# Kernel optimization log

Hardware: AMD Instinct MI355X
Metric: run time of the kernel (lower is better)

The kernel has to match this reference:

```python
import jax, jax.numpy as jnp
import numpy as np

B, S, D, H = 4, 2048, 1024, 16
HD = D // H

def setup_inputs() -> dict:
    key = jax.random.key(0)
    ks = jax.random.split(key, 12)
    std = 1.0 / np.sqrt(D)
    inp = {
        'query': jax.random.normal(ks[0], (B, S, D), jnp.float32),
        'key':   jax.random.normal(ks[1], (B, S, D), jnp.float32),
        'value': jax.random.normal(ks[2], (B, S, D), jnp.float32),
        'mask':  jnp.tril(jnp.ones((S, S), jnp.int32))[None, None, :, :],  # [1,1,S,S] causal
        'Wq': jax.random.uniform(ks[3], (D, D), jnp.float32, -std, std),
        'bq': jax.random.uniform(ks[4], (D,), jnp.float32, -std, std),
        'Wk': jax.random.uniform(ks[5], (D, D), jnp.float32, -std, std),
        'bk': jax.random.uniform(ks[6], (D,), jnp.float32, -std, std),
        'Wv': jax.random.uniform(ks[7], (D, D), jnp.float32, -std, std),
        'bv': jax.random.uniform(ks[8], (D,), jnp.float32, -std, std),
        'Wo': jax.random.uniform(ks[9], (D, D), jnp.float32, -std, std),
        'bo': jax.random.uniform(ks[10], (D,), jnp.float32, -std, std),
    }
    return inp

def _split_heads(x, W, b):
    # torch Linear: x @ W.T + b ; then [B,S,H,HD] -> [B,H,S,HD]
    y = jnp.einsum('bsd,ed->bse', x, W) + b
    return y.reshape(x.shape[0], -1, H, HD).transpose(0, 2, 1, 3)

def reference(query, key, value, mask, Wq, bq, Wk, bk, Wv, bv, Wo, bo):
    q = _split_heads(query, Wq, bq)   # [B,H,S,HD]
    k = _split_heads(key,   Wk, bk)
    v = _split_heads(value, Wv, bv)
    logits = jnp.einsum('bhqd,bhkd->bhqk', q, k) / np.sqrt(HD)  # [B,H,S,S]
    logits = jnp.where(mask == 0, jnp.float32(-1e9), logits)
    attn = jax.nn.softmax(logits, axis=-1)
    out = jnp.einsum('bhqk,bhkd->bhqd', attn, v)               # [B,H,S,HD]
    out = out.transpose(0, 2, 1, 3).reshape(query.shape[0], -1, D)
    return jnp.einsum('bsd,ed->bse', out, Wo) + bo
```

## Files before the change

kernel.cpp:

```cpp
#include <hip/hip_runtime.h>
#include <hip/hip_bf16.h>


#define SLEN 2048
#define DMOD 1024

typedef __attribute__((ext_vector_type(8))) short s16x8;
typedef __attribute__((ext_vector_type(4))) float f32x4;

__device__ __forceinline__ unsigned short f2bf(float f) {
    union { __hip_bfloat16 h; unsigned short u; } cv;
    cv.h = __float2bfloat16(f);
    return cv.u;
}
__device__ __forceinline__ unsigned pack2bf(float a, float b) {
    return (unsigned)f2bf(a) | ((unsigned)f2bf(b) << 16);
}

__device__ __forceinline__ void gload_lds16(const void* g, void* l) {
    __builtin_amdgcn_global_load_lds(
        (const __attribute__((address_space(1))) void*)g,
        (__attribute__((address_space(3))) void*)l, 16, 0, 0);
}

__global__ __launch_bounds__(256) void convert_bf16(
    const float* __restrict__ q, const float* __restrict__ k,
    const float* __restrict__ v, const float* __restrict__ wq,
    const float* __restrict__ wk, const float* __restrict__ wv,
    const float* __restrict__ wo, unsigned short* __restrict__ ws)
{
    const int bid = blockIdx.x, tid = threadIdx.x;
    const float* src;
    unsigned short* dst;
    size_t off;
    if (bid < 3072) {
        const int t = bid >> 10;
        src = (t == 0) ? q : (t == 1) ? k : v;
        dst = ws + (size_t)t * 8388608;
        off = (size_t)(bid & 1023) * 8192;
    } else {
        const int w = (bid - 3072) >> 7;
        src = (w == 0) ? wq : (w == 1) ? wk : (w == 2) ? wv : wo;
        dst = ws + 25165824 + (size_t)w * 1048576;
        off = (size_t)((bid - 3072) & 127) * 8192;
    }
#pragma unroll
    for (int i = 0; i < 8; ++i) {
        const size_t e = off + (size_t)(i * 256 + tid) * 4;
        float4 x = *reinterpret_cast<const float4*>(&src[e]);
        uint2 u;
        u.x = pack2bf(x.x, x.y);
        u.y = pack2bf(x.z, x.w);
        *reinterpret_cast<uint2*>(&dst[e]) = u;
    }
}

template<int MODE>
__global__ __launch_bounds__(256) void gemm_bf16(
    const unsigned short* __restrict__ A, const unsigned short* __restrict__ W,
    const float* __restrict__ bias, void* __restrict__ outp)
{
    __shared__ unsigned short Asm[128 * 64];
    __shared__ unsigned short Bsm[128 * 64];

    const int tid  = threadIdx.x;
    const int lane = tid & 63, wid = tid >> 6;
    const int l15 = lane & 15, lhi = lane >> 4;

    const int flat = blockIdx.x;
    const int logical = (flat & 7) * 64 + (flat >> 3);
    const int m0 = (logical >> 3) * 128, n0 = (logical & 7) * 128;

    const int wr = wid >> 1, wc = wid & 1;
    const int srow = lane >> 3;
    const int sgr  = (lane & 7) ^ srow;

    f32x4 acc[4][4];
#pragma unroll
    for (int i = 0; i < 4; ++i)
#pragma unroll
        for (int j = 0; j < 4; ++j) acc[i][j] = (f32x4)0.f;

#pragma unroll 1
    for (int k0 = 0; k0 < 1024; k0 += 64) {
#pragma unroll
        for (int i = 0; i < 4; ++i) {
            const int rl = i * 32 + wid * 8 + srow;
            gload_lds16(&A[(size_t)(m0 + rl) * 1024 + k0 + sgr * 8],
                        (char*)Asm + i * 4096 + wid * 1024);
            gload_lds16(&W[(size_t)(n0 + rl) * 1024 + k0 + sgr * 8],
                        (char*)Bsm + i * 4096 + wid * 1024);
        }
        __syncthreads();

#pragma unroll
        for (int kk = 0; kk < 2; ++kk) {
            s16x8 af[4], bfv[4];
#pragma unroll
            for (int i = 0; i < 4; ++i) {
                const int row = wr * 64 + i * 16 + l15;
                const int s = (4 * kk + lhi) ^ (l15 & 7);
                af[i] = *reinterpret_cast<const s16x8*>(&Asm[row * 64 + s * 8]);
            }
#pragma unroll
            for (int j = 0; j < 4; ++j) {
                const int row = wc * 64 + j * 16 + l15;
                const int s = (4 * kk + lhi) ^ (l15 & 7);
                bfv[j] = *reinterpret_cast<const s16x8*>(&Bsm[row * 64 + s * 8]);
            }
#pragma unroll
            for (int i = 0; i < 4; ++i)
#pragma unroll
                for (int j = 0; j < 4; ++j)
                    acc[i][j] = __builtin_amdgcn_mfma_f32_16x16x32_bf16(af[i], bfv[j], acc[i][j], 0, 0, 0);
        }
        __syncthreads();
    }

#pragma unroll
    for (int j = 0; j < 4; ++j) {
        const int col = n0 + wc * 64 + j * 16 + l15;
        const float bv = bias[col];
#pragma unroll
        for (int i = 0; i < 4; ++i) {
#pragma unroll
            for (int r = 0; r < 4; ++r) {
                const int row = m0 + wr * 64 + i * 16 + lhi * 4 + r;
                const float val = acc[i][j][r] + bv;
                if constexpr (MODE == 2) {
                    ((float*)outp)[(size_t)row * 1024 + col] = val;
                } else if constexpr (MODE == 0) {
                    ((unsigned short*)outp)[(size_t)((row >> 11) * 16 + (col >> 6)) * 131072
                                            + (size_t)(row & 2047) * 64 + (col & 63)] = f2bf(val);
                } else {
                    ((unsigned short*)outp)[(size_t)((row >> 11) * 16 + (col >> 6)) * 131072
                                            + (size_t)(col & 63) * 2048 + (row & 2047)] = f2bf(val);
                }
            }
        }
    }
}

#define EXPC 0.18033688011112043f

__global__ __launch_bounds__(256, 4) void attn_kernel(
    const unsigned short* __restrict__ Q,
    const unsigned short* __restrict__ Kc,
    const unsigned short* __restrict__ Vt,
    unsigned short* __restrict__ Ao)
{
    __shared__ unsigned short Kbuf[2][4096];
    __shared__ unsigned short Vbuf[2][4096];
    __shared__ unsigned short Psm[4][1024];

    const int tid = threadIdx.x, lane = tid & 63, wid = tid >> 6;
    const int l15 = lane & 15, lhi = lane >> 4;
    const int sK = l15 & 7;
    const int sub = lane >> 3, c8s = lane & 7;

    const int flat = blockIdx.x;
    const int logical = (flat & 7) * 128 + (flat >> 3);
    const int bx = logical & 15, bh = logical >> 4;

    const size_t base = (size_t)bh * SLEN * 64;
    const unsigned short* Qb = Q + base;
    const unsigned short* Kb = Kc + base;
    const unsigned short* Vb = Vt + base;
    const int b = bh >> 4, h = bh & 15;

#pragma unroll 1
    for (int seg = 0; seg < 2; ++seg) {
        const int qt = seg ? (31 - bx) : bx;
        const int q0 = qt * 64;
        const int qrow = q0 + wid * 16 + l15;

        s16x8 aq[2];
#pragma unroll
        for (int kk = 0; kk < 2; ++kk)
            aq[kk] = *reinterpret_cast<const s16x8*>(
                &Qb[(size_t)(q0 + wid * 16 + l15) * 64 + kk * 32 + 8 * lhi]);

        f32x4 o_acc[4];
#pragma unroll
        for (int nb = 0; nb < 4; ++nb) o_acc[nb] = (f32x4)0.f;
        float m_r = -1e30f, l_part = 0.f;

        const int nt = qt + 1;

        auto stage = [&](int tt, int bsel) {
#pragma unroll
            for (int i = 0; i < 2; ++i) {
                const int row = 16 * wid + 8 * i + sub;
                const int col16 = c8s ^ (row & 7);
                gload_lds16(&Kb[(size_t)(tt * 64 + row) * 64 + col16 * 8],
                            (char*)&Kbuf[bsel][0] + wid * 2048 + i * 1024);
                gload_lds16(&Vb[(size_t)row * SLEN + tt * 64 + col16 * 8],
                            (char*)&Vbuf[bsel][0] + wid * 2048 + i * 1024);
            }
        };

        stage(0, 0);
        __syncthreads();

        int cur = 0;
#pragma unroll 1
        for (int t = 0; t < nt; ++t) {
            const int kv0 = t * 64;
            if (t + 1 < nt) stage(t + 1, cur ^ 1);

            const unsigned short* KL = Kbuf[cur];
            const unsigned short* VL = Vbuf[cur];

            f32x4 sc2[4];
#pragma unroll
            for (int nb = 0; nb < 4; ++nb) sc2[nb] = (f32x4)0.f;
            __builtin_amdgcn_s_setprio(1);
#pragma unroll
            for (int kk = 0; kk < 2; ++kk) {
                s16x8 ak[4];
#pragma unroll
                for (int nb = 0; nb < 4; ++nb) {
                    const int g = (nb * 16 + l15) * 8 + ((4 * kk + lhi) ^ sK);
                    ak[nb] = *reinterpret_cast<const s16x8*>(&KL[g * 8]);
                }
#pragma unroll
                for (int nb = 0; nb < 4; ++nb)
                    sc2[nb] = __builtin_amdgcn_mfma_f32_16x16x32_bf16(ak[nb], aq[kk], sc2[nb], 0, 0, 0);
            }
            __builtin_amdgcn_s_setprio(0);

            const bool diag = (kv0 + 63 > q0 + wid * 16);
            float tmx = -3e30f;
#pragma unroll
            for (int nb = 0; nb < 4; ++nb)
#pragma unroll
                for (int r = 0; r < 4; ++r) {
                    float x = sc2[nb][r];
                    if (diag && (kv0 + nb * 16 + lhi * 4 + r > qrow)) x = -3e30f;
                    sc2[nb][r] = x;
                    tmx = fmaxf(tmx, x);
                }

            if (__any(tmx - m_r > 64.0f)) {
                float tf = fmaxf(tmx, __shfl_xor(tmx, 16));
                tf = fmaxf(tf, __shfl_xor(tf, 32));
                const float mn = fmaxf(m_r, tf);
                const float alpha = exp2f((m_r - mn) * EXPC);
                m_r = mn;
                l_part *= alpha;
                float ar[4];
#pragma unroll
                for (int r = 0; r < 4; ++r) ar[r] = __shfl(alpha, lhi * 4 + r);
#pragma unroll
                for (int nb = 0; nb < 4; ++nb)
#pragma unroll
                    for (int r = 0; r < 4; ++r) o_acc[nb][r] *= ar[r];
            }

            const float negmC = -m_r * EXPC;
            unsigned short* Pw = &Psm[wid][0];
#pragma unroll
            for (int nb = 0; nb < 4; ++nb) {
                float p0 = exp2f(fmaf(sc2[nb][0], EXPC, negmC));
                float p1 = exp2f(fmaf(sc2[nb][1], EXPC, negmC));
                float p2 = exp2f(fmaf(sc2[nb][2], EXPC, negmC));
                float p3 = exp2f(fmaf(sc2[nb][3], EXPC, negmC));
                l_part += (p0 + p1) + (p2 + p3);
                uint2 u;
                u.x = pack2bf(p0, p1);
                u.y = pack2bf(p2, p3);
                const int g8 = l15 * 16 + ((nb * 4 + lhi) ^ (2 * sK));
                *reinterpret_cast<uint2*>(&Pw[g8 * 4]) = u;
            }

            __builtin_amdgcn_s_setprio(1);
#pragma unroll
            for (int kk = 0; kk < 2; ++kk) {
                const int gp = l15 * 8 + ((4 * kk + lhi) ^ sK);
                s16x8 pa = *reinterpret_cast<const s16x8*>(&Pw[gp * 8]);
                s16x8 bvv[4];
#pragma unroll
                for (int nb = 0; nb < 4; ++nb) {
                    const int g = (nb * 16 + l15) * 8 + ((4 * kk + lhi) ^ sK);
                    bvv[nb] = *reinterpret_cast<const s16x8*>(&VL[g * 8]);
                }
#pragma unroll
                for (int nb = 0; nb < 4; ++nb)
                    o_acc[nb] = __builtin_amdgcn_mfma_f32_16x16x32_bf16(pa, bvv[nb], o_acc[nb], 0, 0, 0);
            }
            __builtin_amdgcn_s_setprio(0);

            __syncthreads();
            cur ^= 1;
        }

        float lf = l_part + __shfl_xor(l_part, 16);
        lf += __shfl_xor(lf, 32);
        float linv[4];
#pragma unroll
        for (int r = 0; r < 4; ++r)
            linv[r] = 1.0f / __shfl(lf, lhi * 4 + r);
#pragma unroll
        for (int nb = 0; nb < 4; ++nb)
#pragma unroll
            for (int r = 0; r < 4; ++r) {
                const int s = q0 + wid * 16 + lhi * 4 + r;
                Ao[((size_t)b * SLEN + s) * DMOD + h * 64 + nb * 16 + l15] =
                    f2bf(o_acc[nb][r] * linv[r]);
            }
        if (seg == 0) __syncthreads();
    }
}

extern "C" void kernel_launch(void* const* d_in, const int* in_sizes, int n_in,
                              void* d_out, int out_size, void* d_ws, size_t ws_size,
                              hipStream_t stream) {
    const float* q  = (const float*)d_in[0];
    const float* k  = (const float*)d_in[1];
    const float* v  = (const float*)d_in[2];
    const float* Wq = (const float*)d_in[4];
    const float* bq = (const float*)d_in[5];
    const float* Wk = (const float*)d_in[6];
    const float* bk = (const float*)d_in[7];
    const float* Wv = (const float*)d_in[8];
    const float* bv = (const float*)d_in[9];
    const float* Wo = (const float*)d_in[10];
    const float* bo = (const float*)d_in[11];

    unsigned short* wsp = (unsigned short*)d_ws;
    unsigned short* qc  = wsp;
    unsigned short* kc  = wsp + 8388608;
    unsigned short* vc  = wsp + 16777216;
    unsigned short* wqc = wsp + 25165824;
    unsigned short* wkc = wsp + 26214400;
    unsigned short* wvc = wsp + 27262976;
    unsigned short* woc = wsp + 28311552;
    unsigned short* qb  = wsp + 29360128;
    unsigned short* kb  = wsp + 37748736;
    unsigned short* vtb = wsp + 46137344;
    unsigned short* ao  = qc;

    dim3 gb(256);
    convert_bf16<<<dim3(3584), gb, 0, stream>>>(q, k, v, Wq, Wk, Wv, Wo, wsp);
    gemm_bf16<0><<<dim3(512), gb, 0, stream>>>(qc, wqc, bq, qb);
    gemm_bf16<0><<<dim3(512), gb, 0, stream>>>(kc, wkc, bk, kb);
    gemm_bf16<1><<<dim3(512), gb, 0, stream>>>(vc, wvc, bv, vtb);
    attn_kernel<<<dim3(1024), gb, 0, stream>>>(qb, kb, vtb, ao);
    gemm_bf16<2><<<dim3(512), gb, 0, stream>>>(ao, woc, bo, (float*)d_out);
}
```

Measured before the change: 206.5 us.

## Double-buffer GEMM LDS tiles and peel diagonal tile in attention loop

The GEMM kernel gets double-buffered LDS tiles, so the global-to-LDS load for the next K tile is issued before the MFMAs on the current one, and it keeps one barrier per iteration. The LDS offsets in both kernels are precomputed once and the global pointers are advanced incrementally, which removes per-iteration address arithmetic. The attention loop peels the last (diagonal) KV tile so only that tile runs the causal masking. Doubling LDS in the GEMM to 64KB may reduce occupancy, and the extra precomputed offset registers add register pressure.

```diff
diff --git a/kernel.cpp b/kernel.cpp
--- a/kernel.cpp
+++ b/kernel.cpp
@@ -60,8 +60,8 @@
     const unsigned short* __restrict__ A, const unsigned short* __restrict__ W,
     const float* __restrict__ bias, void* __restrict__ outp)
 {
-    __shared__ unsigned short Asm[128 * 64];
-    __shared__ unsigned short Bsm[128 * 64];
+    __shared__ unsigned short Asm[2][8192];
+    __shared__ unsigned short Bsm[2][8192];
 
     const int tid  = threadIdx.x;
     const int lane = tid & 63, wid = tid >> 6;
@@ -75,39 +75,51 @@
     const int srow = lane >> 3;
     const int sgr  = (lane & 7) ^ srow;
 
+    int aoff[2][4], boff[2][4];
+#pragma unroll
+    for (int kk = 0; kk < 2; ++kk)
+#pragma unroll
+        for (int i = 0; i < 4; ++i) {
+            const int s = ((4 * kk + lhi) ^ (l15 & 7)) * 16;
+            aoff[kk][i] = (wr * 64 + i * 16 + l15) * 128 + s;
+            boff[kk][i] = (wc * 64 + i * 16 + l15) * 128 + s;
+        }
+
+    const unsigned short* apt = A + (size_t)(m0 + wid * 8 + srow) * 1024 + sgr * 8;
+    const unsigned short* bpt = W + (size_t)(n0 + wid * 8 + srow) * 1024 + sgr * 8;
+
     f32x4 acc[4][4];
 #pragma unroll
     for (int i = 0; i < 4; ++i)
 #pragma unroll
         for (int j = 0; j < 4; ++j) acc[i][j] = (f32x4)0.f;
 
+    auto stage = [&](int bsel) {
+        char* ad = (char*)Asm + bsel * 16384 + wid * 1024;
+        char* bd = (char*)Bsm + bsel * 16384 + wid * 1024;
+#pragma unroll
+        for (int i = 0; i < 4; ++i) {
+            gload_lds16(apt + i * 32768, ad + i * 4096);
+            gload_lds16(bpt + i * 32768, bd + i * 4096);
+        }
+        apt += 64; bpt += 64;
+    };
+
+    stage(0);
+    __syncthreads();
+    int cur = 0;
 #pragma unroll 1
-    for (int k0 = 0; k0 < 1024; k0 += 64) {
-#pragma unroll
-        for (int i = 0; i < 4; ++i) {
-            const int rl = i * 32 + wid * 8 + srow;
-            gload_lds16(&A[(size_t)(m0 + rl) * 1024 + k0 + sgr * 8],
-                        (char*)Asm + i * 4096 + wid * 1024);
-            gload_lds16(&W[(size_t)(n0 + rl) * 1024 + k0 + sgr * 8],
-                        (char*)Bsm + i * 4096 + wid * 1024);
-        }
-        __syncthreads();
-
+    for (int kt = 0; kt < 16; ++kt) {
+        if (kt < 15) stage(cur ^ 1);
+        const char* AB = (const char*)Asm + cur * 16384;
+        const char* BB = (const char*)Bsm + cur * 16384;
 #pragma unroll
         for (int kk = 0; kk < 2; ++kk) {
             s16x8 af[4], bfv[4];
 #pragma unroll
-            for (int i = 0; i < 4; ++i) {
-                const int row = wr * 64 + i * 16 + l15;
-                const int s = (4 * kk + lhi) ^ (l15 & 7);
-                af[i] = *reinterpret_cast<const s16x8*>(&Asm[row * 64 + s * 8]);
-            }
-#pragma unroll
-            for (int j = 0; j < 4; ++j) {
-                const int row = wc * 64 + j * 16 + l15;
-                const int s = (4 * kk + lhi) ^ (l15 & 7);
-                bfv[j] = *reinterpret_cast<const s16x8*>(&Bsm[row * 64 + s * 8]);
-            }
+            for (int i = 0; i < 4; ++i) af[i]  = *reinterpret_cast<const s16x8*>(AB + aoff[kk][i]);
+#pragma unroll
+            for (int j = 0; j < 4; ++j) bfv[j] = *reinterpret_cast<const s16x8*>(BB + boff[kk][j]);
 #pragma unroll
             for (int i = 0; i < 4; ++i)
 #pragma unroll
@@ -115,6 +127,7 @@
                     acc[i][j] = __builtin_amdgcn_mfma_f32_16x16x32_bf16(af[i], bfv[j], acc[i][j], 0, 0, 0);
         }
         __syncthreads();
+        cur ^= 1;
     }
 
 #pragma unroll
@@ -157,6 +170,19 @@
     const int l15 = lane & 15, lhi = lane >> 4;
     const int sK = l15 & 7;
     const int sub = lane >> 3, c8s = lane & 7;
+    const int thr = wid * 16 + l15;
+
+    int ko[8], pr[2], pw[4];
+#pragma unroll
+    for (int kk = 0; kk < 2; ++kk) {
+        pr[kk] = (l15 * 8 + ((4 * kk + lhi) ^ sK)) * 16;
+#pragma unroll
+        for (int nb = 0; nb < 4; ++nb)
+            ko[kk * 4 + nb] = ((nb * 16 + l15) * 8 + ((4 * kk + lhi) ^ sK)) * 16;
+    }
+#pragma unroll
+    for (int nb = 0; nb < 4; ++nb)
+        pw[nb] = (l15 * 16 + ((nb * 4 + lhi) ^ (2 * sK))) * 8;
 
     const int flat = blockIdx.x;
     const int logical = (flat & 7) * 128 + (flat >> 3);
@@ -167,12 +193,12 @@
     const unsigned short* Kb = Kc + base;
     const unsigned short* Vb = Vt + base;
     const int b = bh >> 4, h = bh & 15;
+    const int scol = (c8s ^ sub) * 8;
 
 #pragma unroll 1
     for (int seg = 0; seg < 2; ++seg) {
         const int qt = seg ? (31 - bx) : bx;
         const int q0 = qt * 64;
-        const int qrow = q0 + wid * 16 + l15;
 
         s16x8 aq[2];
 #pragma unroll
@@ -185,31 +211,23 @@
         for (int nb = 0; nb < 4; ++nb) o_acc[nb] = (f32x4)0.f;
         float m_r = -1e30f, l_part = 0.f;
 
-        const int nt = qt + 1;
-
-        auto stage = [&](int tt, int bsel) {
-#pragma unroll
-            for (int i = 0; i < 2; ++i) {
-                const int row = 16 * wid + 8 * i + sub;
-                const int col16 = c8s ^ (row & 7);
-                gload_lds16(&Kb[(size_t)(tt * 64 + row) * 64 + col16 * 8],
-                            (char*)&Kbuf[bsel][0] + wid * 2048 + i * 1024);
-                gload_lds16(&Vb[(size_t)row * SLEN + tt * 64 + col16 * 8],
-                            (char*)&Vbuf[bsel][0] + wid * 2048 + i * 1024);
-            }
+        const unsigned short* kpt = Kb + (16 * wid + sub) * 64 + scol;
+        const unsigned short* vpt = Vb + (size_t)(16 * wid + sub) * SLEN + scol;
+
+        auto stage = [&](int bsel) {
+            char* kd = (char*)Kbuf + bsel * 8192 + wid * 2048;
+            char* vd = (char*)Vbuf + bsel * 8192 + wid * 2048;
+            gload_lds16(kpt,         kd);
+            gload_lds16(kpt + 512,   kd + 1024);
+            gload_lds16(vpt,         vd);
+            gload_lds16(vpt + 16384, vd + 1024);
+            kpt += 4096; vpt += 64;
         };
 
-        stage(0, 0);
-        __syncthreads();
-
-        int cur = 0;
-#pragma unroll 1
-        for (int t = 0; t < nt; ++t) {
-            const int kv0 = t * 64;
-            if (t + 1 < nt) stage(t + 1, cur ^ 1);
-
-            const unsigned short* KL = Kbuf[cur];
-            const unsigned short* VL = Vbuf[cur];
+        auto tile = [&](int cbo, bool domask) {
+            const char* KB = (const char*)Kbuf + cbo;
+            const char* VB = (const char*)Vbuf + cbo;
+            char* PW = (char*)Psm + wid * 2048;
 
             f32x4 sc2[4];
 #pragma unroll
@@ -219,24 +237,21 @@
             for (int kk = 0; kk < 2; ++kk) {
                 s16x8 ak[4];
 #pragma unroll
-                for (int nb = 0; nb < 4; ++nb) {
-                    const int g = (nb * 16 + l15) * 8 + ((4 * kk + lhi) ^ sK);
-                    ak[nb] = *reinterpret_cast<const s16x8*>(&KL[g * 8]);
-                }
+                for (int nb = 0; nb < 4; ++nb)
+                    ak[nb] = *reinterpret_cast<const s16x8*>(KB + ko[kk * 4 + nb]);
 #pragma unroll
                 for (int nb = 0; nb < 4; ++nb)
                     sc2[nb] = __builtin_amdgcn_mfma_f32_16x16x32_bf16(ak[nb], aq[kk], sc2[nb], 0, 0, 0);
             }
             __builtin_amdgcn_s_setprio(0);
 
-            const bool diag = (kv0 + 63 > q0 + wid * 16);
             float tmx = -3e30f;
 #pragma unroll
             for (int nb = 0; nb < 4; ++nb)
 #pragma unroll
                 for (int r = 0; r < 4; ++r) {
                     float x = sc2[nb][r];
-                    if (diag && (kv0 + nb * 16 + lhi * 4 + r > qrow)) x = -3e30f;
+                    if (domask && (nb * 16 + lhi * 4 + r > thr)) x = -3e30f;
                     sc2[nb][r] = x;
                     tmx = fmaxf(tmx, x);
                 }
@@ -258,7 +273,6 @@
             }
 
             const float negmC = -m_r * EXPC;
-            unsigned short* Pw = &Psm[wid][0];
 #pragma unroll
             for (int nb = 0; nb < 4; ++nb) {
                 float p0 = exp2f(fmaf(sc2[nb][0], EXPC, negmC));
@@ -269,30 +283,36 @@
                 uint2 u;
                 u.x = pack2bf(p0, p1);
                 u.y = pack2bf(p2, p3);
-                const int g8 = l15 * 16 + ((nb * 4 + lhi) ^ (2 * sK));
-                *reinterpret_cast<uint2*>(&Pw[g8 * 4]) = u;
+                *reinterpret_cast<uint2*>(PW + pw[nb]) = u;
             }
 
             __builtin_amdgcn_s_setprio(1);
 #pragma unroll
             for (int kk = 0; kk < 2; ++kk) {
-                const int gp = l15 * 8 + ((4 * kk + lhi) ^ sK);
-                s16x8 pa = *reinterpret_cast<const s16x8*>(&Pw[gp * 8]);
+                s16x8 pa = *reinterpret_cast<const s16x8*>(PW + pr[kk]);
                 s16x8 bvv[4];
 #pragma unroll
-                for (int nb = 0; nb < 4; ++nb) {
-                    const int g = (nb * 16 + l15) * 8 + ((4 * kk + lhi) ^ sK);
-                    bvv[nb] = *reinterpret_cast<const s16x8*>(&VL[g * 8]);
-                }
+                for (int nb = 0; nb < 4; ++nb)
+                    bvv[nb] = *reinterpret_cast<const s16x8*>(VB + ko[kk * 4 + nb]);
 #pragma unroll
                 for (int nb = 0; nb < 4; ++nb)
                     o_acc[nb] = __builtin_amdgcn_mfma_f32_16x16x32_bf16(pa, bvv[nb], o_acc[nb], 0, 0, 0);
             }
             __builtin_amdgcn_s_setprio(0);
-
+        };
+
+        stage(0);
+        __syncthreads();
+        int cur = 0;
+
+#pragma unroll 1
+        for (int t = 0; t < qt; ++t) {
+            stage(cur ^ 1);
+            tile(cur * 8192, false);
             __syncthreads();
             cur ^= 1;
         }
+        tile(cur * 8192, true);
 
         float lf = l_part + __shfl_xor(l_part, 16);
         lf += __shfl_xor(lf, 32);
@@ -308,7 +328,7 @@
                 Ao[((size_t)b * SLEN + s) * DMOD + h * 64 + nb * 16 + l15] =
                     f2bf(o_acc[nb][r] * linv[r]);
             }
-        if (seg == 0) __syncthreads();
+        __syncthreads();
     }
 }
 
```

Result: faster. 190.5 us (-7.8%).
